# Optimization experiments

Hardware: AMD Instinct MI355X
Metric: run time of the kernel (lower is better)

## Reference

```python
import jax, jax.numpy as jnp
import numpy as np

B, C, N, K, C_OUT = 16, 64, 2048, 3, 64


def setup_inputs() -> dict:
    key = jax.random.key(0)
    k1, k2, k3 = jax.random.split(key, 3)
    x = jax.random.normal(k1, (B, C, N), dtype=jnp.float32)
    # Conv1d params: weight [out_ch, in_ch, K], bias [out_ch]
    fan_in = C * K
    bound = 1.0 / np.sqrt(fan_in)
    W = jax.random.uniform(k2, (C_OUT, C, K), dtype=jnp.float32, minval=-bound, maxval=bound)
    b = jax.random.uniform(k3, (C_OUT,), dtype=jnp.float32, minval=-bound, maxval=bound)
    return {"x": x, "W": W, "b": b}


def reference(x, W, b):
    # x: [B, C, N]
    # pairwise squared-distance matrix over the length dim: [B, N, N]
    norm_sq = jnp.sum(x * x, axis=1, keepdims=True)              # [B, 1, N]
    dot = jnp.einsum('bcn,bcm->bnm', x, x)                       # [B, N, N]
    dist = norm_sq + jnp.swapaxes(norm_sq, 1, 2) - 2.0 * dot     # [B, N, N]
    # K smallest distances per point (self included, dist=0)
    _, idx = jax.lax.top_k(-dist, K)                             # [B, N, K]
    # gather neighbors: prime[b, c, n*K + k] = x[b, c, idx[b, n, k]]
    idx_flat = idx.reshape(B, 1, N * K)
    prime = jnp.take_along_axis(x, jnp.broadcast_to(idx_flat, (B, C, N * K)), axis=2)
    # Conv1d(kernel=K, stride=K, padding=0) -> [B, C_OUT, N]
    out = jax.lax.conv_general_dilated(
        prime, W, window_strides=(K,), padding='VALID',
        dimension_numbers=('NCH', 'OIH', 'NCH'))
    out = out + b[None, :, None]
    return jax.nn.relu(out)
```

## Files before the change

### kernel.cpp

```cpp
#include <hip/hip_runtime.h>
#include <float.h>

#define BB 16
#define CC 64
#define NN 2048
#define KNN 3
#define COUT 64
#define SPL 4

typedef _Float16 half8 __attribute__((ext_vector_type(8)));
typedef float f32x16 __attribute__((ext_vector_type(16)));

__global__ __launch_bounds__(256) void k_prep(const float* __restrict__ x,
                                              uint4* __restrict__ xe,
                                              unsigned* __restrict__ anc) {
    __shared__ float t[64][65];
    __shared__ float nsh[64];
    const int b = blockIdx.x;
    const int n0 = blockIdx.y * 64;
    const int tid = threadIdx.x;
    const int ln = tid & 63, g = tid >> 6;
#pragma unroll
    for (int i = 0; i < 16; ++i) {
        const int c = g + 4 * i;
        t[c][ln] = x[((size_t)b * CC + c) * NN + n0 + ln];
    }
    __syncthreads();
    if (tid < 64) {
        float s = 0.f;
#pragma unroll
        for (int c = 0; c < 64; ++c) s = fmaf(t[c][tid], t[c][tid], s);
        nsh[tid] = s;
    }
#pragma unroll
    for (int i = 0; i < 4; ++i) {
        const int cid = tid + 256 * i;
        const int lane = cid & 63;
        const int kblk = (cid >> 6) & 7;
        const int ctl = cid >> 9;
        const int m = ctl * 32 + (lane & 31);
        const int khalf = (lane >> 5) * 8;
        union { uint4 v; _Float16 h[8]; } pk;
#pragma unroll
        for (int j = 0; j < 8; ++j) {
            const int kg = kblk * 16 + khalf + j;
            const int ch = kg & 63;
            const float f = t[ch][m];
            const _Float16 hi = (_Float16)f;
            pk.h[j] = (kg < 64) ? hi : (_Float16)(f - (float)hi);
        }
        const int ct = (n0 >> 5) + ctl;
        xe[((size_t)(b * 64 + ct) * 8 + kblk) * 64 + lane] = pk.v;
    }
    __syncthreads();
    if (tid < 128) {
        const int ctl = tid >> 6, l = tid & 63;
        const int ct = (n0 >> 5) + ctl;
        unsigned v = 0;
        if (l < 32) {
            const float h = -0.5f * nsh[ctl * 32 + l];
            const _Float16 a0 = (_Float16)h;
            const _Float16 a1 = (_Float16)(h - (float)a0);
            union { unsigned u; _Float16 hh[2]; } cu;
            cu.hh[0] = a0; cu.hh[1] = a1;
            v = cu.u;
        }
        anc[(size_t)(b * 64 + ct) * 64 + l] = v;
    }
}

__global__ __launch_bounds__(256) void k_wprep(const float* __restrict__ W,
                                               uint4* __restrict__ Wf) {
    const int tid = threadIdx.x;
#pragma unroll
    for (int i = 0; i < 6; ++i) {
        const int id = tid + 256 * i;
        const int l = id & 63;
        const int kb = (id >> 6) & 3;
        const int ct2 = (id >> 8) & 1;
        const int kk = id >> 9;
        const int co = ct2 * 32 + (l & 31);
        union { uint4 v; _Float16 h[8]; } pk;
#pragma unroll
        for (int j = 0; j < 8; ++j) {
            const int c = kb * 16 + 8 * (l >> 5) + j;
            pk.h[j] = (_Float16)W[(co * CC + c) * KNN + kk];
        }
        Wf[id] = pk.v;
    }
}

__global__ __launch_bounds__(256, 4) void k_top3(const half8* __restrict__ xe,
                                                 const unsigned* __restrict__ anc,
                                                 float* __restrict__ pd,
                                                 int* __restrict__ pi) {
    const int tid = threadIdx.x;
    const int lane = tid & 63;
    const int qg = blockIdx.x * 4 + (tid >> 6);
    const int s = blockIdx.y;
    const int b = blockIdx.z;

    half8 bq[8];
#pragma unroll
    for (int kb = 0; kb < 8; ++kb)
        bq[kb] = xe[((size_t)(b * 64 + qg) * 8 + kb) * 64 + lane];

    half8 bnc = {};
    if (lane < 32) { bnc[0] = (_Float16)1.0f; bnc[1] = (_Float16)1.0f; }

    float k0 = -FLT_MAX, k1 = -FLT_MAX, k2 = -FLT_MAX;
    int i0 = -1, i1 = -1, i2 = -1;
    const int hi4 = (lane >> 5) * 4;

    const int ct0 = s * (NN / 32 / SPL);
    for (int t = 0; t < NN / 32 / SPL; ++t) {
        const int ct = ct0 + t;
        half8 af[8];
#pragma unroll
        for (int kb = 0; kb < 8; ++kb)
            af[kb] = xe[((size_t)(b * 64 + ct) * 8 + kb) * 64 + lane];
        half8 av = {};
        {
            union { unsigned u; _Float16 hh[2]; } cu;
            cu.u = anc[(size_t)(b * 64 + ct) * 64 + lane];
            av[0] = cu.hh[0]; av[1] = cu.hh[1];
        }
        f32x16 acc = {};
#pragma unroll
        for (int kb = 0; kb < 8; ++kb)
            acc = __builtin_amdgcn_mfma_f32_32x32x16_f16(af[kb], bq[kb], acc, 0, 0, 0);
#pragma unroll
        for (int kb = 0; kb < 8; ++kb)
            acc = __builtin_amdgcn_mfma_f32_32x32x16_f16(af[kb], bq[(kb + 4) & 7], acc, 0, 0, 0);
        acc = __builtin_amdgcn_mfma_f32_32x32x16_f16(av, bnc, acc, 0, 0, 0);

        const int mbase = ct * 32 + hi4;
#pragma unroll
        for (int j = 0; j < 16; ++j) {
            const float a = acc[j];
            if (__any(a > k2)) {
                const int m = mbase + (j & 3) + 8 * (j >> 2);
                const bool g0 = a > k0, g1 = a > k1, g2 = a > k2;
                k2 = g1 ? k1 : (g2 ? a : k2); i2 = g1 ? i1 : (g2 ? m : i2);
                k1 = g0 ? k0 : (g1 ? a : k1); i1 = g0 ? i0 : (g1 ? m : i1);
                k0 = g0 ? a : k0;             i0 = g0 ? m : i0;
            }
        }
    }

    const float ok[3] = {__shfl_xor(k0, 32), __shfl_xor(k1, 32), __shfl_xor(k2, 32)};
    const int oi[3] = {__shfl_xor(i0, 32), __shfl_xor(i1, 32), __shfl_xor(i2, 32)};
#pragma unroll
    for (int r = 0; r < 3; ++r) {
        const float ck = ok[r]; const int ci = oi[r];
        const bool b0 = (ck > k0) || (ck == k0 && ci < i0);
        const bool b1 = (ck > k1) || (ck == k1 && ci < i1);
        const bool b2 = (ck > k2) || (ck == k2 && ci < i2);
        k2 = b1 ? k1 : (b2 ? ck : k2); i2 = b1 ? i1 : (b2 ? ci : i2);
        k1 = b0 ? k0 : (b1 ? ck : k1); i1 = b0 ? i0 : (b1 ? ci : i1);
        k0 = b0 ? ck : k0;             i0 = b0 ? ci : i0;
    }
    if (lane < 32) {
        const int q = qg * 32 + lane;
        const size_t o = (((size_t)b * SPL + s) * NN + q) * 3;
        pd[o] = -2.0f * k0; pd[o + 1] = -2.0f * k1; pd[o + 2] = -2.0f * k2;
        pi[o] = i0; pi[o + 1] = i1; pi[o + 2] = i2;
    }
}

__global__ __launch_bounds__(256) void k_merge(const float* __restrict__ pd,
                                               const int* __restrict__ pi,
                                               int* __restrict__ fi) {
    const int t = blockIdx.x * 256 + threadIdx.x;
    if (t >= BB * NN) return;
    const int b = t / NN, n = t % NN;
    float dv[3 * SPL]; int iv[3 * SPL];
#pragma unroll
    for (int s = 0; s < SPL; ++s) {
        const size_t o = (((size_t)b * SPL + s) * NN + n) * 3;
#pragma unroll
        for (int r = 0; r < 3; ++r) {
            dv[s * 3 + r] = pd[o + r];
            iv[s * 3 + r] = pi[o + r];
        }
    }
    float bd = -FLT_MAX; int bi = -1;
#pragma unroll
    for (int r = 0; r < 3; ++r) {
        float cd = FLT_MAX; int ci = 0x7fffffff;
#pragma unroll
        for (int j = 0; j < 3 * SPL; ++j) {
            const bool gt_prev = (dv[j] > bd) || (dv[j] == bd && iv[j] > bi);
            const bool lt_cur = (dv[j] < cd) || (dv[j] == cd && iv[j] < ci);
            if (gt_prev && lt_cur) { cd = dv[j]; ci = iv[j]; }
        }
        fi[(size_t)t * 3 + r] = ci;
        bd = cd; bi = ci;
    }
}

__global__ __launch_bounds__(256) void k_conv(const uint4* __restrict__ xe,
                                              const uint4* __restrict__ Wf,
                                              const int* __restrict__ fi,
                                              const float* __restrict__ bias,
                                              float* __restrict__ out) {
    __shared__ float ot[64][65];
    const int b = blockIdx.y;
    const int n0 = blockIdx.x * 64;
    const int tid = threadIdx.x;
    const int l = tid & 63;
    const int w = tid >> 6;
    const int mt = w >> 1, ct2 = w & 1;
    const int p31 = l & 31, kh = l >> 5;
    const int npt = n0 + mt * 32 + p31;

    f32x16 acc = {};
    const uint4* xb = xe + (size_t)b * 64 * 8 * 64;
    const int fbase3 = (b * NN + npt) * KNN;
#pragma unroll
    for (int kk = 0; kk < KNN; ++kk) {
        const int src = fi[fbase3 + kk];
        const uint4* ap = xb + (size_t)(src >> 5) * 512 + (src & 31) + 32 * kh;
        uint4 af[4], bw[4];
#pragma unroll
        for (int kb = 0; kb < 4; ++kb) af[kb] = ap[(size_t)kb * 64];
#pragma unroll
        for (int kb = 0; kb < 4; ++kb) bw[kb] = Wf[((kk * 2 + ct2) * 4 + kb) * 64 + l];
#pragma unroll
        for (int kb = 0; kb < 4; ++kb) {
            union { uint4 v; half8 h; } ua, ub;
            ua.v = af[kb]; ub.v = bw[kb];
            acc = __builtin_amdgcn_mfma_f32_32x32x16_f16(ua.h, ub.h, acc, 0, 0, 0);
        }
    }
    const int co = ct2 * 32 + p31;
    const float bv = bias[co];
#pragma unroll
    for (int j = 0; j < 16; ++j) {
        const int pt = mt * 32 + (j & 3) + 8 * (j >> 2) + 4 * kh;
        ot[co][pt] = fmaxf(acc[j] + bv, 0.f);
    }
    __syncthreads();
#pragma unroll
    for (int i = 0; i < 16; ++i) {
        const int v = tid + 256 * i;
        const int co2 = v >> 6, col = v & 63;
        out[((size_t)(b * COUT + co2)) * NN + n0 + col] = ot[co2][col];
    }
}

extern "C" void kernel_launch(void* const* d_in, const int* in_sizes, int n_in,
                              void* d_out, int out_size, void* d_ws, size_t ws_size,
                              hipStream_t stream) {
    const float* x = (const float*)d_in[0];
    const float* W = (const float*)d_in[1];
    const float* bias = (const float*)d_in[2];
    float* out = (float*)d_out;

    char* ws = (char*)d_ws;
    uint4* xe = (uint4*)(ws);
    unsigned* anc = (unsigned*)(ws + 8388608);
    uint4* Wf = (uint4*)(ws + 8650752);
    float* pd = (float*)(ws + 8675328);
    int* pi = (int*)(ws + 10248192);
    int* fi = (int*)(ws + 11821056);

    k_prep<<<dim3(BB, NN / 64), 256, 0, stream>>>(x, xe, anc);
    k_wprep<<<1, 256, 0, stream>>>(W, Wf);
    k_top3<<<dim3(16, SPL, BB), 256, 0, stream>>>((const half8*)xe, anc, pd, pi);
    k_merge<<<(BB * NN + 255) / 256, 256, 0, stream>>>(pd, pi, fi);
    k_conv<<<dim3(NN / 64, BB), 256, 0, stream>>>(xe, Wf, fi, bias, out);
}
```

Before: 78.11 us.

## Process two query tiles per wave in top-3 and pack partial results

```diff
diff --git a/kernel.cpp b/kernel.cpp
--- a/kernel.cpp
+++ b/kernel.cpp
@@ -6,7 +6,7 @@
 #define NN 2048
 #define KNN 3
 #define COUT 64
-#define SPL 4
+#define SPL 8
 
 typedef _Float16 half8 __attribute__((ext_vector_type(8)));
 typedef float f32x16 __attribute__((ext_vector_type(16)));
@@ -53,19 +53,15 @@
         xe[((size_t)(b * 64 + ct) * 8 + kblk) * 64 + lane] = pk.v;
     }
     __syncthreads();
-    if (tid < 128) {
-        const int ctl = tid >> 6, l = tid & 63;
+    if (tid < 64) {
+        const int ctl = tid >> 5, l = tid & 31;
         const int ct = (n0 >> 5) + ctl;
-        unsigned v = 0;
-        if (l < 32) {
-            const float h = -0.5f * nsh[ctl * 32 + l];
-            const _Float16 a0 = (_Float16)h;
-            const _Float16 a1 = (_Float16)(h - (float)a0);
-            union { unsigned u; _Float16 hh[2]; } cu;
-            cu.hh[0] = a0; cu.hh[1] = a1;
-            v = cu.u;
-        }
-        anc[(size_t)(b * 64 + ct) * 64 + l] = v;
+        const float h = -0.5f * nsh[ctl * 32 + l];
+        const _Float16 a0 = (_Float16)h;
+        const _Float16 a1 = (_Float16)(h - (float)a0);
+        union { unsigned u; _Float16 hh[2]; } cu;
+        cu.hh[0] = a0; cu.hh[1] = a1;
+        anc[(size_t)(b * 64 + ct) * 32 + l] = cu.u;
     }
 }
 
@@ -90,30 +86,34 @@
     }
 }
 
-__global__ __launch_bounds__(256, 4) void k_top3(const half8* __restrict__ xe,
+__global__ __launch_bounds__(256, 2) void k_top3(const half8* __restrict__ xe,
                                                  const unsigned* __restrict__ anc,
-                                                 float* __restrict__ pd,
-                                                 int* __restrict__ pi) {
+                                                 uint4* __restrict__ pk) {
     const int tid = threadIdx.x;
     const int lane = tid & 63;
-    const int qg = blockIdx.x * 4 + (tid >> 6);
+    const int wq = blockIdx.x * 4 + (tid >> 6);
+    const int qgA = wq * 2, qgB = wq * 2 + 1;
     const int s = blockIdx.y;
     const int b = blockIdx.z;
 
-    half8 bq[8];
-#pragma unroll
-    for (int kb = 0; kb < 8; ++kb)
-        bq[kb] = xe[((size_t)(b * 64 + qg) * 8 + kb) * 64 + lane];
-
+    half8 bqA[8], bqB[8];
+#pragma unroll
+    for (int kb = 0; kb < 8; ++kb) {
+        bqA[kb] = xe[((size_t)(b * 64 + qgA) * 8 + kb) * 64 + lane];
+        bqB[kb] = xe[((size_t)(b * 64 + qgB) * 8 + kb) * 64 + lane];
+    }
     half8 bnc = {};
     if (lane < 32) { bnc[0] = (_Float16)1.0f; bnc[1] = (_Float16)1.0f; }
 
-    float k0 = -FLT_MAX, k1 = -FLT_MAX, k2 = -FLT_MAX;
-    int i0 = -1, i1 = -1, i2 = -1;
+    float kA0 = -FLT_MAX, kA1 = -FLT_MAX, kA2 = -FLT_MAX;
+    float kB0 = -FLT_MAX, kB1 = -FLT_MAX, kB2 = -FLT_MAX;
+    int iA0 = -1, iA1 = -1, iA2 = -1;
+    int iB0 = -1, iB1 = -1, iB2 = -1;
     const int hi4 = (lane >> 5) * 4;
 
-    const int ct0 = s * (NN / 32 / SPL);
-    for (int t = 0; t < NN / 32 / SPL; ++t) {
+    constexpr int TILES = NN / 32 / SPL;
+    const int ct0 = s * TILES;
+    for (int t = 0; t < TILES; ++t) {
         const int ct = ct0 + t;
         half8 af[8];
 #pragma unroll
@@ -122,54 +122,79 @@
         half8 av = {};
         {
             union { unsigned u; _Float16 hh[2]; } cu;
-            cu.u = anc[(size_t)(b * 64 + ct) * 64 + lane];
+            cu.u = anc[(size_t)(b * 64 + ct) * 32 + (lane & 31)];
             av[0] = cu.hh[0]; av[1] = cu.hh[1];
         }
-        f32x16 acc = {};
-#pragma unroll
-        for (int kb = 0; kb < 8; ++kb)
-            acc = __builtin_amdgcn_mfma_f32_32x32x16_f16(af[kb], bq[kb], acc, 0, 0, 0);
-#pragma unroll
-        for (int kb = 0; kb < 8; ++kb)
-            acc = __builtin_amdgcn_mfma_f32_32x32x16_f16(af[kb], bq[(kb + 4) & 7], acc, 0, 0, 0);
-        acc = __builtin_amdgcn_mfma_f32_32x32x16_f16(av, bnc, acc, 0, 0, 0);
-
-        const int mbase = ct * 32 + hi4;
+        f32x16 accA = {}, accB = {};
+#pragma unroll
+        for (int kb = 0; kb < 8; ++kb) {
+            accA = __builtin_amdgcn_mfma_f32_32x32x16_f16(af[kb], bqA[kb], accA, 0, 0, 0);
+            accB = __builtin_amdgcn_mfma_f32_32x32x16_f16(af[kb], bqB[kb], accB, 0, 0, 0);
+        }
+#pragma unroll
+        for (int kb = 0; kb < 8; ++kb) {
+            accA = __builtin_amdgcn_mfma_f32_32x32x16_f16(af[kb], bqA[(kb + 4) & 7], accA, 0, 0, 0);
+            accB = __builtin_amdgcn_mfma_f32_32x32x16_f16(af[kb], bqB[(kb + 4) & 7], accB, 0, 0, 0);
+        }
+        accA = __builtin_amdgcn_mfma_f32_32x32x16_f16(av, bnc, accA, 0, 0, 0);
+        accB = __builtin_amdgcn_mfma_f32_32x32x16_f16(av, bnc, accB, 0, 0, 0);
+
+        const int mbase = t * 32 + hi4;
 #pragma unroll
         for (int j = 0; j < 16; ++j) {
-            const float a = acc[j];
-            if (__any(a > k2)) {
+            const float a = accA[j];
+            if (__any(a > kA2)) {
                 const int m = mbase + (j & 3) + 8 * (j >> 2);
-                const bool g0 = a > k0, g1 = a > k1, g2 = a > k2;
-                k2 = g1 ? k1 : (g2 ? a : k2); i2 = g1 ? i1 : (g2 ? m : i2);
-                k1 = g0 ? k0 : (g1 ? a : k1); i1 = g0 ? i0 : (g1 ? m : i1);
-                k0 = g0 ? a : k0;             i0 = g0 ? m : i0;
+                const bool g0 = a > kA0, g1 = a > kA1, g2 = a > kA2;
+                kA2 = g1 ? kA1 : (g2 ? a : kA2); iA2 = g1 ? iA1 : (g2 ? m : iA2);
+                kA1 = g0 ? kA0 : (g1 ? a : kA1); iA1 = g0 ? iA0 : (g1 ? m : iA1);
+                kA0 = g0 ? a : kA0;              iA0 = g0 ? m : iA0;
             }
         }
-    }
-
-    const float ok[3] = {__shfl_xor(k0, 32), __shfl_xor(k1, 32), __shfl_xor(k2, 32)};
-    const int oi[3] = {__shfl_xor(i0, 32), __shfl_xor(i1, 32), __shfl_xor(i2, 32)};
-#pragma unroll
-    for (int r = 0; r < 3; ++r) {
-        const float ck = ok[r]; const int ci = oi[r];
-        const bool b0 = (ck > k0) || (ck == k0 && ci < i0);
-        const bool b1 = (ck > k1) || (ck == k1 && ci < i1);
-        const bool b2 = (ck > k2) || (ck == k2 && ci < i2);
-        k2 = b1 ? k1 : (b2 ? ck : k2); i2 = b1 ? i1 : (b2 ? ci : i2);
-        k1 = b0 ? k0 : (b1 ? ck : k1); i1 = b0 ? i0 : (b1 ? ci : i1);
-        k0 = b0 ? ck : k0;             i0 = b0 ? ci : i0;
-    }
-    if (lane < 32) {
-        const int q = qg * 32 + lane;
-        const size_t o = (((size_t)b * SPL + s) * NN + q) * 3;
-        pd[o] = -2.0f * k0; pd[o + 1] = -2.0f * k1; pd[o + 2] = -2.0f * k2;
-        pi[o] = i0; pi[o + 1] = i1; pi[o + 2] = i2;
-    }
-}
-
-__global__ __launch_bounds__(256) void k_merge(const float* __restrict__ pd,
-                                               const int* __restrict__ pi,
+#pragma unroll
+        for (int j = 0; j < 16; ++j) {
+            const float a = accB[j];
+            if (__any(a > kB2)) {
+                const int m = mbase + (j & 3) + 8 * (j >> 2);
+                const bool g0 = a > kB0, g1 = a > kB1, g2 = a > kB2;
+                kB2 = g1 ? kB1 : (g2 ? a : kB2); iB2 = g1 ? iB1 : (g2 ? m : iB2);
+                kB1 = g0 ? kB0 : (g1 ? a : kB1); iB1 = g0 ? iB0 : (g1 ? m : iB1);
+                kB0 = g0 ? a : kB0;              iB0 = g0 ? m : iB0;
+            }
+        }
+    }
+
+#pragma unroll
+    for (int grp = 0; grp < 2; ++grp) {
+        float K0 = grp ? kB0 : kA0, K1 = grp ? kB1 : kA1, K2 = grp ? kB2 : kA2;
+        int I0 = grp ? iB0 : iA0, I1 = grp ? iB1 : iA1, I2 = grp ? iB2 : iA2;
+        const float ok0 = __shfl_xor(K0, 32), ok1 = __shfl_xor(K1, 32), ok2 = __shfl_xor(K2, 32);
+        const int oi0 = __shfl_xor(I0, 32), oi1 = __shfl_xor(I1, 32), oi2 = __shfl_xor(I2, 32);
+        const float ck[3] = {ok0, ok1, ok2};
+        const int cix[3] = {oi0, oi1, oi2};
+#pragma unroll
+        for (int r = 0; r < 3; ++r) {
+            const float c = ck[r]; const int ci = cix[r];
+            const bool b0 = (c > K0) || (c == K0 && ci < I0);
+            const bool b1 = (c > K1) || (c == K1 && ci < I1);
+            const bool b2 = (c > K2) || (c == K2 && ci < I2);
+            K2 = b1 ? K1 : (b2 ? c : K2); I2 = b1 ? I1 : (b2 ? ci : I2);
+            K1 = b0 ? K0 : (b1 ? c : K1); I1 = b0 ? I0 : (b1 ? ci : I1);
+            K0 = b0 ? c : K0;             I0 = b0 ? ci : I0;
+        }
+        if (lane < 32) {
+            const int q = (grp ? qgB : qgA) * 32 + lane;
+            uint4 v;
+            v.x = __float_as_uint(K0);
+            v.y = __float_as_uint(K1);
+            v.z = __float_as_uint(K2);
+            v.w = (unsigned)I0 | ((unsigned)I1 << 8) | ((unsigned)I2 << 16);
+            pk[((size_t)b * SPL + s) * NN + q] = v;
+        }
+    }
+}
+
+__global__ __launch_bounds__(256) void k_merge(const uint4* __restrict__ pk,
                                                int* __restrict__ fi) {
     const int t = blockIdx.x * 256 + threadIdx.x;
     if (t >= BB * NN) return;
@@ -177,25 +202,26 @@
     float dv[3 * SPL]; int iv[3 * SPL];
 #pragma unroll
     for (int s = 0; s < SPL; ++s) {
-        const size_t o = (((size_t)b * SPL + s) * NN + n) * 3;
-#pragma unroll
-        for (int r = 0; r < 3; ++r) {
-            dv[s * 3 + r] = pd[o + r];
-            iv[s * 3 + r] = pi[o + r];
-        }
-    }
-    float bd = -FLT_MAX; int bi = -1;
+        const uint4 v = pk[((size_t)b * SPL + s) * NN + n];
+        dv[s * 3 + 0] = __uint_as_float(v.x);
+        dv[s * 3 + 1] = __uint_as_float(v.y);
+        dv[s * 3 + 2] = __uint_as_float(v.z);
+        iv[s * 3 + 0] = (int)(v.w & 255u) + s * 256;
+        iv[s * 3 + 1] = (int)((v.w >> 8) & 255u) + s * 256;
+        iv[s * 3 + 2] = (int)((v.w >> 16) & 255u) + s * 256;
+    }
+    float bd = FLT_MAX; int bi = -1;
 #pragma unroll
     for (int r = 0; r < 3; ++r) {
-        float cd = FLT_MAX; int ci = 0x7fffffff;
+        float ck = -FLT_MAX; int ci = 0x7fffffff;
 #pragma unroll
         for (int j = 0; j < 3 * SPL; ++j) {
-            const bool gt_prev = (dv[j] > bd) || (dv[j] == bd && iv[j] > bi);
-            const bool lt_cur = (dv[j] < cd) || (dv[j] == cd && iv[j] < ci);
-            if (gt_prev && lt_cur) { cd = dv[j]; ci = iv[j]; }
+            const bool after_prev = (dv[j] < bd) || (dv[j] == bd && iv[j] > bi);
+            const bool better = (dv[j] > ck) || (dv[j] == ck && iv[j] < ci);
+            if (after_prev && better) { ck = dv[j]; ci = iv[j]; }
         }
         fi[(size_t)t * 3 + r] = ci;
-        bd = cd; bi = ci;
+        bd = ck; bi = ci;
     }
 }
 
@@ -260,14 +286,13 @@
     char* ws = (char*)d_ws;
     uint4* xe = (uint4*)(ws);
     unsigned* anc = (unsigned*)(ws + 8388608);
-    uint4* Wf = (uint4*)(ws + 8650752);
-    float* pd = (float*)(ws + 8675328);
-    int* pi = (int*)(ws + 10248192);
-    int* fi = (int*)(ws + 11821056);
+    uint4* Wf = (uint4*)(ws + 8519680);
+    uint4* pk = (uint4*)(ws + 8544256);
+    int* fi = (int*)(ws + 12738560);
 
     k_prep<<<dim3(BB, NN / 64), 256, 0, stream>>>(x, xe, anc);
     k_wprep<<<1, 256, 0, stream>>>(W, Wf);
-    k_top3<<<dim3(16, SPL, BB), 256, 0, stream>>>((const half8*)xe, anc, pd, pi);
-    k_merge<<<(BB * NN + 255) / 256, 256, 0, stream>>>(pd, pi, fi);
+    k_top3<<<dim3(8, SPL, BB), 256, 0, stream>>>((const half8*)xe, anc, pk);
+    k_merge<<<(BB * NN + 255) / 256, 256, 0, stream>>>(pk, fi);
     k_conv<<<dim3(NN / 64, BB), 256, 0, stream>>>(xe, Wf, fi, bias, out);
 }
```

After: 81.54 us. +4.4%, slower.
